# Kernel tuning notes

Measured on AMD Instinct MI355X. Metric: run time of the kernel, lower is better.

Reference implementation:

```python
import jax, jax.numpy as jnp
import numpy as np

NUM_BINS_X = 128; NUM_BINS_Y = 128
XL, XH, YL, YH = 0.0, 1000.0, 0.0, 1000.0
NUM_NETS = 100000
NUM_NODES = 200000
NUM_MOVABLE = 180000
NUM_PINS = 400000
UNIT_H_CAP = 1.5
UNIT_V_CAP = 1.4
MAX_RATE = 2.0
MIN_RATE = 1.0 / MAX_RATE
BIN_SX = (XH - XL) / NUM_BINS_X
BIN_SY = (YH - YL) / NUM_BINS_Y


def setup_inputs() -> dict:
    key = jax.random.key(0)
    k1, k2, k3, k4, k5, k6, k7, k8 = jax.random.split(key, 8)
    pos = jnp.concatenate([
        jax.random.uniform(k1, (NUM_NODES,), jnp.float32, XL, XH - 8.0),
        jax.random.uniform(k2, (NUM_NODES,), jnp.float32, YL, YH - 8.0)])
    pin_pos = jnp.concatenate([
        jax.random.uniform(k3, (NUM_PINS,), jnp.float32, XL, XH),
        jax.random.uniform(k4, (NUM_PINS,), jnp.float32, YL, YH)])
    node_size_x = jax.random.uniform(k5, (NUM_NODES,), jnp.float32, 1.0, 8.0)
    node_size_y = jax.random.uniform(k6, (NUM_NODES,), jnp.float32, 1.0, 8.0)
    # 4 pins per net (uniform ragged layout); flat_netpin is a permutation of pins
    netpin_start = jnp.arange(NUM_NETS + 1, dtype=jnp.int32) * (NUM_PINS // NUM_NETS)
    flat_netpin = jax.random.permutation(k7, NUM_PINS).astype(jnp.int32)
    net_weights = jax.random.uniform(k8, (NUM_NETS,), jnp.float32, 0.5, 1.5)
    return dict(pos=pos, pin_pos=pin_pos, node_size_x=node_size_x,
                node_size_y=node_size_y, net_weights=net_weights,
                netpin_start=netpin_start, flat_netpin=flat_netpin)


def _bin_edges(lo, size, n):
    l = lo + jnp.arange(n, dtype=jnp.float32) * size
    return l, l + size


def _overlap(lo_e, hi_e, lo, hi):
    # per-interval overlap of [lo, hi] with each bin [lo_e, hi_e]; >=0
    return jnp.clip(jnp.minimum(hi_e[None, :], hi[:, None]) -
                    jnp.maximum(lo_e[None, :], lo[:, None]), 0.0, None)


def reference(pos, pin_pos, node_size_x, node_size_y, net_weights,
              netpin_start, flat_netpin):
    # ---- phase 1: per-net bbox (ragged gather) + RUDY demand binning ----
    lengths = netpin_start[1:] - netpin_start[:-1]                      # [N]
    net_ids = jnp.repeat(jnp.arange(NUM_NETS, dtype=jnp.int32), lengths,
                         total_repeat_length=NUM_PINS)                  # [P]
    px = pin_pos[flat_netpin]
    py = pin_pos[flat_netpin + NUM_PINS]
    x_min = jax.ops.segment_min(px, net_ids, num_segments=NUM_NETS)
    x_max = jax.ops.segment_max(px, net_ids, num_segments=NUM_NETS)
    y_min = jax.ops.segment_min(py, net_ids, num_segments=NUM_NETS)
    y_max = jax.ops.segment_max(py, net_ids, num_segments=NUM_NETS)

    bxl, bxr = _bin_edges(XL, BIN_SX, NUM_BINS_X)
    byl, byr = _bin_edges(YL, BIN_SY, NUM_BINS_Y)
    ox = _overlap(bxl, bxr, x_min, x_max)                               # [N, BX]
    oy = _overlap(byl, byr, y_min, y_max)                               # [N, BY]
    dx = x_max - x_min
    dy = y_max - y_min
    # horizontal demand per bin = wt * overlap / (y_max - y_min); vertical analog
    cx = jnp.where(dy > 0, net_weights / jnp.where(dy > 0, dy, 1.0), 0.0)
    cy = jnp.where(dx > 0, net_weights / jnp.where(dx > 0, dx, 1.0), 0.0)
    map_x = jnp.einsum('nx,ny->xy', ox * cx[:, None], oy)               # [BX, BY]
    map_y = jnp.einsum('nx,ny->xy', ox * cy[:, None], oy)

    bin_area = BIN_SX * BIN_SY
    ux = map_x / (bin_area * UNIT_H_CAP)
    uy = map_y / (bin_area * UNIT_V_CAP)
    util = jnp.clip(jnp.maximum(ux, uy), MIN_RATE, MAX_RATE)            # [BX, BY]

    # ---- phase 2: per movable node, overlap-weighted utilization read-back ----
    nx = pos[:NUM_MOVABLE]
    ny = pos[NUM_NODES:NUM_NODES + NUM_MOVABLE]
    sx = node_size_x[:NUM_MOVABLE]
    sy = node_size_y[:NUM_MOVABLE]
    oxn = _overlap(bxl, bxr, nx, nx + sx)                               # [M, BX]
    oyn = _overlap(byl, byr, ny, ny + sy)                               # [M, BY]
    tmp = jnp.einsum('mx,xy->my', oxn, util)                            # [M, BY]
    instance_route_area = jnp.sum(tmp * oyn, axis=1)                    # [M]
    return instance_route_area
```

## Files before the change

kernel.cpp:

```cpp
#include <hip/hip_runtime.h>

constexpr int   NB         = 128;
constexpr int   NCELL      = NB * NB;
constexpr int   NFL        = 2 * NCELL;
constexpr float S          = 7.8125f;
constexpr int   NUM_NETS   = 100000;
constexpr int   NUM_NODES  = 200000;
constexpr int   NUM_MOVABLE= 180000;
constexpr int   NUM_PINS   = 400000;
constexpr float UNIT_H_CAP = 1.5f;
constexpr float UNIT_V_CAP = 1.4f;

#define TPB    1024
#define NDB    256
#define NCHUNK 8

__device__ __forceinline__ float edgef(int t) { return (float)t * S; }

__device__ __forceinline__ int bin_of(float v) {
    int t = (int)floorf(v / S);
    while (edgef(t + 1) <= v) ++t;
    while (edgef(t)     >  v) --t;
    return t;
}

__device__ __forceinline__ float phi(int t, float lo, float hi) {
    return fminf(fmaxf(edgef(t), lo), hi);
}

__device__ __forceinline__ int second_diff(float lo, float hi,
                                           int* idx, float* val) {
    int a = bin_of(lo);
    int b = bin_of(hi);
    int n = 0;
    idx[n] = a;
    val[n] = phi(a + 1, lo, hi) - 2.f * phi(a, lo, hi) + phi(a - 1, lo, hi);
    ++n;
    idx[n] = a + 1;
    val[n] = phi(a + 2, lo, hi) - 2.f * phi(a + 1, lo, hi) + phi(a, lo, hi);
    ++n;
    if (b > a + 1) {
        idx[n] = b;
        val[n] = phi(b + 1, lo, hi) - 2.f * phi(b, lo, hi) + phi(b - 1, lo, hi);
        ++n;
    }
    if (b > a) {
        idx[n] = b + 1;
        val[n] = phi(b + 2, lo, hi) - 2.f * phi(b + 1, lo, hi) + phi(b, lo, hi);
        ++n;
    }
    return n;
}

__global__ __launch_bounds__(TPB) void net_diff_kernel(
    const float* __restrict__ pin_pos,
    const float* __restrict__ net_weights,
    const int*   __restrict__ nps,
    const int*   __restrict__ fnp,
    float* __restrict__ P) {
    extern __shared__ float Dl[];
    const int tid = threadIdx.x;

    float4* D4 = (float4*)Dl;
    for (int i = tid; i < NFL / 4; i += TPB) D4[i] = make_float4(0, 0, 0, 0);
    __syncthreads();

    const int per = (NUM_NETS + gridDim.x - 1) / gridDim.x;
    const int n0  = blockIdx.x * per;
    const int n1  = min(n0 + per, NUM_NETS);

    for (int n = n0 + tid; n < n1; n += TPB) {
        int s = nps[n], e = nps[n + 1];
        if (e <= s) continue;
        float xmin, xmax, ymin, ymax;
        if (e - s == 4 && (s & 3) == 0) {
            int4 p4 = *(const int4*)(fnp + s);
            float x0 = pin_pos[p4.x], y0 = pin_pos[p4.x + NUM_PINS];
            float x1 = pin_pos[p4.y], y1 = pin_pos[p4.y + NUM_PINS];
            float x2 = pin_pos[p4.z], y2 = pin_pos[p4.z + NUM_PINS];
            float x3 = pin_pos[p4.w], y3 = pin_pos[p4.w + NUM_PINS];
            xmin = fminf(fminf(x0, x1), fminf(x2, x3));
            xmax = fmaxf(fmaxf(x0, x1), fmaxf(x2, x3));
            ymin = fminf(fminf(y0, y1), fminf(y2, y3));
            ymax = fmaxf(fmaxf(y0, y1), fmaxf(y2, y3));
        } else {
            xmin = 1e30f; xmax = -1e30f; ymin = 1e30f; ymax = -1e30f;
            for (int p = s; p < e; ++p) {
                int pin = fnp[p];
                float px = pin_pos[pin];
                float py = pin_pos[pin + NUM_PINS];
                xmin = fminf(xmin, px); xmax = fmaxf(xmax, px);
                ymin = fminf(ymin, py); ymax = fmaxf(ymax, py);
            }
        }
        float w  = net_weights[n];
        float dx = xmax - xmin, dy = ymax - ymin;
        float cx = (dy > 0.f) ? w / dy : 0.f;
        float cy = (dx > 0.f) ? w / dx : 0.f;
        if (cx == 0.f && cy == 0.f) continue;

        int ixs[4], iys[4];
        float vxs[4], vys[4];
        int nx = second_diff(xmin, xmax, ixs, vxs);
        int ny = second_diff(ymin, ymax, iys, vys);

        for (int i = 0; i < nx; ++i) {
            int row = ixs[i];
            float fi = vxs[i];
            if (fi == 0.f || row >= NB) continue;
            for (int j = 0; j < ny; ++j) {
                int col = iys[j];
                float t = fi * vys[j];
                if (t == 0.f || col >= NB) continue;
                int cell = row * NB + col;
                if (cx != 0.f) atomicAdd(&Dl[cell],         cx * t);
                if (cy != 0.f) atomicAdd(&Dl[NCELL + cell], cy * t);
            }
        }
    }
    __syncthreads();

    float4* Pb = (float4*)(P + (size_t)blockIdx.x * NFL);
    for (int i = tid; i < NFL / 4; i += TPB) Pb[i] = D4[i];
}

__global__ __launch_bounds__(256) void reduce_kernel(
    const float4* __restrict__ P,
    float4* __restrict__ Rc,
    int B) {
    constexpr int NF4 = NFL / 4;
    int g = blockIdx.y * blockDim.x + threadIdx.x;
    int chunk = blockIdx.x;
    float4 a0 = {0,0,0,0}, a1 = {0,0,0,0}, a2 = {0,0,0,0}, a3 = {0,0,0,0};
    int b = chunk;
    for (; b + 3 * NCHUNK < B; b += 4 * NCHUNK) {
        float4 v0 = P[(size_t)(b             ) * NF4 + g];
        float4 v1 = P[(size_t)(b +     NCHUNK) * NF4 + g];
        float4 v2 = P[(size_t)(b + 2 * NCHUNK) * NF4 + g];
        float4 v3 = P[(size_t)(b + 3 * NCHUNK) * NF4 + g];
        a0.x += v0.x; a0.y += v0.y; a0.z += v0.z; a0.w += v0.w;
        a1.x += v1.x; a1.y += v1.y; a1.z += v1.z; a1.w += v1.w;
        a2.x += v2.x; a2.y += v2.y; a2.z += v2.z; a2.w += v2.w;
        a3.x += v3.x; a3.y += v3.y; a3.z += v3.z; a3.w += v3.w;
    }
    for (; b < B; b += NCHUNK) {
        float4 v = P[(size_t)b * NF4 + g];
        a0.x += v.x; a0.y += v.y; a0.z += v.z; a0.w += v.w;
    }
    float4 r;
    r.x = (a0.x + a1.x) + (a2.x + a3.x);
    r.y = (a0.y + a1.y) + (a2.y + a3.y);
    r.z = (a0.z + a1.z) + (a2.z + a3.z);
    r.w = (a0.w + a1.w) + (a2.w + a3.w);
    Rc[(size_t)chunk * NF4 + g] = r;
}

__global__ __launch_bounds__(NB) void scan_x_kernel(
    const float* __restrict__ Rc,
    float2* __restrict__ Xp) {
    __shared__ float2 sm[NB];
    int col = blockIdx.x;
    int t = threadIdx.x;
    int idx = t * NB + col;
    float2 v = make_float2(0.f, 0.f);
    #pragma unroll
    for (int c = 0; c < NCHUNK; ++c) {
        v.x += Rc[(size_t)c * NFL + idx];
        v.y += Rc[(size_t)c * NFL + NCELL + idx];
    }
    sm[t] = v;
    __syncthreads();
    #pragma unroll
    for (int off = 1; off < NB; off <<= 1) {
        float2 cur = sm[t];
        float2 add = (t >= off) ? sm[t - off] : make_float2(0.f, 0.f);
        __syncthreads();
        cur.x += add.x; cur.y += add.y;
        sm[t] = cur;
        __syncthreads();
    }
    Xp[idx] = sm[t];
}

__global__ __launch_bounds__(NB) void scan_y_kernel(
    const float2* __restrict__ Xp,
    float* __restrict__ util) {
    __shared__ float2 sm[NB];
    int row = blockIdx.x;
    int t = threadIdx.x;
    sm[t] = Xp[row * NB + t];
    __syncthreads();
    #pragma unroll
    for (int off = 1; off < NB; off <<= 1) {
        float2 cur = sm[t];
        float2 add = (t >= off) ? sm[t - off] : make_float2(0.f, 0.f);
        __syncthreads();
        cur.x += add.x; cur.y += add.y;
        sm[t] = cur;
        __syncthreads();
    }
    constexpr float invx = 1.f / (S * S * UNIT_H_CAP);
    constexpr float invy = 1.f / (S * S * UNIT_V_CAP);
    float2 r = sm[t];
    float u = fmaxf(r.x * invx, r.y * invy);
    util[row * NB + t] = fminf(fmaxf(u, 0.5f), 2.0f);
}

__global__ __launch_bounds__(256) void node_kernel(
    const float* __restrict__ pos,
    const float* __restrict__ nsx,
    const float* __restrict__ nsy,
    const float* __restrict__ util,
    float* __restrict__ out) {
    int m = blockIdx.x * blockDim.x + threadIdx.x;
    if (m >= NUM_MOVABLE) return;
    float x  = pos[m];
    float y  = pos[NUM_NODES + m];
    float xh = x + nsx[m];
    float yh = y + nsy[m];
    int ax = max(0,      (int)floorf(x  / S) - 1);
    int bx = min(NB - 1, (int)floorf(xh / S) + 1);
    int ay = max(0,      (int)floorf(y  / S) - 1);
    int by = min(NB - 1, (int)floorf(yh / S) + 1);
    float acc = 0.f;
    for (int i = ax; i <= bx; ++i) {
        float ov = fminf(edgef(i + 1), xh) - fmaxf(edgef(i), x);
        if (ov <= 0.f) continue;
        float inner = 0.f;
        for (int j = ay; j <= by; ++j) {
            float ovy = fminf(edgef(j + 1), yh) - fmaxf(edgef(j), y);
            if (ovy > 0.f) inner += ovy * util[i * NB + j];
        }
        acc += ov * inner;
    }
    out[m] = acc;
}

extern "C" void kernel_launch(void* const* d_in, const int* in_sizes, int n_in,
                              void* d_out, int out_size, void* d_ws, size_t ws_size,
                              hipStream_t stream) {
    const float* pos      = (const float*)d_in[0];
    const float* pin_pos  = (const float*)d_in[1];
    const float* nsx      = (const float*)d_in[2];
    const float* nsy      = (const float*)d_in[3];
    const float* nw       = (const float*)d_in[4];
    const int*   npstart  = (const int*)d_in[5];
    const int*   fnp      = (const int*)d_in[6];
    float*       out      = (float*)d_out;

    float* w    = (float*)d_ws;
    float* Rc   = w;                           w += NCHUNK * NFL;
    float* Xp   = w;                           w += NFL;
    float* util = w;                           w += NCELL;
    float* P    = w;

    size_t fixed = (size_t)(w - (float*)d_ws) * sizeof(float);
    int B = NDB;
    if (ws_size > fixed) {
        size_t fit = (ws_size - fixed) / ((size_t)NFL * sizeof(float));
        if ((size_t)B > fit) B = (int)fit;
    } else {
        B = 1;
    }
    if (B < 1) B = 1;

    (void)hipFuncSetAttribute((const void*)net_diff_kernel,
                              hipFuncAttributeMaxDynamicSharedMemorySize,
                              NFL * (int)sizeof(float));

    net_diff_kernel<<<B, TPB, NFL * sizeof(float), stream>>>(
        pin_pos, nw, npstart, fnp, P);
    {
        dim3 g(NCHUNK, NFL / 4 / 256);
        reduce_kernel<<<g, 256, 0, stream>>>(
            (const float4*)P, (float4*)Rc, B);
    }
    scan_x_kernel<<<NB, NB, 0, stream>>>(Rc, (float2*)Xp);
    scan_y_kernel<<<NB, NB, 0, stream>>>((const float2*)Xp, util);
    node_kernel<<<(NUM_MOVABLE + 255) / 256, 256, 0, stream>>>(
        pos, nsx, nsy, util, out);
}
```

Baseline: 116.2 us.

## Split each net across four lanes for pin gather and row scatter

Measured after the change: 115.0 us. Within noise of the previous version (-1.0%).

```diff
diff --git a/kernel.cpp b/kernel.cpp
--- a/kernel.cpp
+++ b/kernel.cpp
@@ -28,30 +28,6 @@
     return fminf(fmaxf(edgef(t), lo), hi);
 }
 
-__device__ __forceinline__ int second_diff(float lo, float hi,
-                                           int* idx, float* val) {
-    int a = bin_of(lo);
-    int b = bin_of(hi);
-    int n = 0;
-    idx[n] = a;
-    val[n] = phi(a + 1, lo, hi) - 2.f * phi(a, lo, hi) + phi(a - 1, lo, hi);
-    ++n;
-    idx[n] = a + 1;
-    val[n] = phi(a + 2, lo, hi) - 2.f * phi(a + 1, lo, hi) + phi(a, lo, hi);
-    ++n;
-    if (b > a + 1) {
-        idx[n] = b;
-        val[n] = phi(b + 1, lo, hi) - 2.f * phi(b, lo, hi) + phi(b - 1, lo, hi);
-        ++n;
-    }
-    if (b > a) {
-        idx[n] = b + 1;
-        val[n] = phi(b + 2, lo, hi) - 2.f * phi(b + 1, lo, hi) + phi(b, lo, hi);
-        ++n;
-    }
-    return n;
-}
-
 __global__ __launch_bounds__(TPB) void net_diff_kernel(
     const float* __restrict__ pin_pos,
     const float* __restrict__ net_weights,
@@ -68,54 +44,74 @@
     const int per = (NUM_NETS + gridDim.x - 1) / gridDim.x;
     const int n0  = blockIdx.x * per;
     const int n1  = min(n0 + per, NUM_NETS);
-
-    for (int n = n0 + tid; n < n1; n += TPB) {
+    const int l   = tid & 3;
+    const int g   = tid >> 2;
+    constexpr int GP = TPB / 4;
+
+    for (int n = n0 + g; n < n1; n += GP) {
         int s = nps[n], e = nps[n + 1];
-        if (e <= s) continue;
+        bool ok = (e > s);
         float xmin, xmax, ymin, ymax;
-        if (e - s == 4 && (s & 3) == 0) {
-            int4 p4 = *(const int4*)(fnp + s);
-            float x0 = pin_pos[p4.x], y0 = pin_pos[p4.x + NUM_PINS];
-            float x1 = pin_pos[p4.y], y1 = pin_pos[p4.y + NUM_PINS];
-            float x2 = pin_pos[p4.z], y2 = pin_pos[p4.z + NUM_PINS];
-            float x3 = pin_pos[p4.w], y3 = pin_pos[p4.w + NUM_PINS];
-            xmin = fminf(fminf(x0, x1), fminf(x2, x3));
-            xmax = fmaxf(fmaxf(x0, x1), fmaxf(x2, x3));
-            ymin = fminf(fminf(y0, y1), fminf(y2, y3));
-            ymax = fmaxf(fmaxf(y0, y1), fmaxf(y2, y3));
+        if (ok && (e - s == 4)) {
+            int pin = fnp[s + l];
+            float xv = pin_pos[pin];
+            float yv = pin_pos[pin + NUM_PINS];
+            xmin = xv; xmax = xv; ymin = yv; ymax = yv;
         } else {
             xmin = 1e30f; xmax = -1e30f; ymin = 1e30f; ymax = -1e30f;
-            for (int p = s; p < e; ++p) {
-                int pin = fnp[p];
-                float px = pin_pos[pin];
-                float py = pin_pos[pin + NUM_PINS];
-                xmin = fminf(xmin, px); xmax = fmaxf(xmax, px);
-                ymin = fminf(ymin, py); ymax = fmaxf(ymax, py);
+            if (ok && l == 0) {
+                for (int p = s; p < e; ++p) {
+                    int pin = fnp[p];
+                    float px = pin_pos[pin];
+                    float py = pin_pos[pin + NUM_PINS];
+                    xmin = fminf(xmin, px); xmax = fmaxf(xmax, px);
+                    ymin = fminf(ymin, py); ymax = fmaxf(ymax, py);
+                }
             }
         }
+        xmin = fminf(xmin, __shfl_xor(xmin, 1));
+        xmin = fminf(xmin, __shfl_xor(xmin, 2));
+        xmax = fmaxf(xmax, __shfl_xor(xmax, 1));
+        xmax = fmaxf(xmax, __shfl_xor(xmax, 2));
+        ymin = fminf(ymin, __shfl_xor(ymin, 1));
+        ymin = fminf(ymin, __shfl_xor(ymin, 2));
+        ymax = fmaxf(ymax, __shfl_xor(ymax, 1));
+        ymax = fmaxf(ymax, __shfl_xor(ymax, 2));
+        if (!ok) continue;
+
         float w  = net_weights[n];
         float dx = xmax - xmin, dy = ymax - ymin;
         float cx = (dy > 0.f) ? w / dy : 0.f;
         float cy = (dx > 0.f) ? w / dx : 0.f;
         if (cx == 0.f && cy == 0.f) continue;
 
-        int ixs[4], iys[4];
-        float vxs[4], vys[4];
-        int nx = second_diff(xmin, xmax, ixs, vxs);
-        int ny = second_diff(ymin, ymax, iys, vys);
-
-        for (int i = 0; i < nx; ++i) {
-            int row = ixs[i];
-            float fi = vxs[i];
-            if (fi == 0.f || row >= NB) continue;
-            for (int j = 0; j < ny; ++j) {
-                int col = iys[j];
-                float t = fi * vys[j];
-                if (t == 0.f || col >= NB) continue;
-                int cell = row * NB + col;
-                if (cx != 0.f) atomicAdd(&Dl[cell],         cx * t);
-                if (cy != 0.f) atomicAdd(&Dl[NCELL + cell], cy * t);
-            }
+        int ax = bin_of(xmin), bx = bin_of(xmax);
+        int row; bool has;
+        if      (l == 0) { row = ax;     has = true; }
+        else if (l == 1) { row = ax + 1; has = true; }
+        else if (l == 2) { row = bx;     has = (bx > ax + 1); }
+        else             { row = bx + 1; has = (bx > ax); }
+        if (!has || row >= NB) continue;
+        float fi = phi(row + 1, xmin, xmax) - 2.f * phi(row, xmin, xmax)
+                 + phi(row - 1, xmin, xmax);
+        if (fi == 0.f) continue;
+
+        int ay = bin_of(ymin), by = bin_of(ymax);
+        #pragma unroll
+        for (int j = 0; j < 4; ++j) {
+            int col; bool hj;
+            if      (j == 0) { col = ay;     hj = true; }
+            else if (j == 1) { col = ay + 1; hj = true; }
+            else if (j == 2) { col = by;     hj = (by > ay + 1); }
+            else             { col = by + 1; hj = (by > ay); }
+            if (!hj || col >= NB) continue;
+            float fj = phi(col + 1, ymin, ymax) - 2.f * phi(col, ymin, ymax)
+                     + phi(col - 1, ymin, ymax);
+            float t = fi * fj;
+            if (t == 0.f) continue;
+            int cell = row * NB + col;
+            if (cx != 0.f) atomicAdd(&Dl[cell],         cx * t);
+            if (cy != 0.f) atomicAdd(&Dl[NCELL + cell], cy * t);
         }
     }
     __syncthreads();
```
